# Kernel tuning notes

Measured on AMD Instinct MI355X. Metric: run time of the kernel, lower is better.

## Reference

```python
import jax, jax.numpy as jnp
from jax import lax
import numpy as np

V, D_EMB, H, P, B, T = 32000, 512, 1024, 512, 32, 512
NUM_LAYERS = 2


def setup_inputs() -> dict:
    key = jax.random.key(0)
    ks = jax.random.split(key, 2 + NUM_LAYERS * 5)
    tokens = jax.random.randint(ks[0], (B, T), 0, V, dtype=jnp.int32)
    embed = jax.random.normal(ks[1], (V, D_EMB), dtype=jnp.float32) * 0.02
    inp = {"tokens": tokens, "embed": embed}
    in_dims = [D_EMB] + [P] * (NUM_LAYERS - 1)
    for l in range(NUM_LAYERS):
        kk = ks[2 + 5 * l: 7 + 5 * l]
        inp[f"Wx{l}"] = jax.random.normal(kk[0], (in_dims[l], 4 * H), dtype=jnp.float32) * 0.02
        inp[f"Wh{l}"] = jax.random.normal(kk[1], (H, 4 * H), dtype=jnp.float32) * 0.02
        inp[f"b{l}"] = jnp.zeros((4 * H,), dtype=jnp.float32)
        inp[f"Wfc{l}"] = jax.random.normal(kk[3], (H, P), dtype=jnp.float32) * 0.02
        inp[f"bfc{l}"] = jnp.zeros((P,), dtype=jnp.float32)
    return inp


def _lstm(x, Wx, Wh, b):
    # x: [B, T, D] -> [B, T, H]. Keras gate order: i, f, g(cell), o.
    Bsz = x.shape[0]
    h0 = jnp.zeros((Bsz, H), dtype=x.dtype)
    c0 = jnp.zeros((Bsz, H), dtype=x.dtype)

    # Precompute input projection for all timesteps (one big GEMM).
    xz = jnp.einsum('btd,dg->btg', x, Wx) + b  # [B, T, 4H]

    def step(carry, zt):
        h, c = carry
        z = zt + h @ Wh
        i, f, g, o = jnp.split(z, 4, axis=-1)
        c = jax.nn.sigmoid(f) * c + jax.nn.sigmoid(i) * jnp.tanh(g)
        h = jax.nn.sigmoid(o) * jnp.tanh(c)
        return (h, c), h

    _, ys = lax.scan(step, (h0, c0), jnp.swapaxes(xz, 0, 1))  # ys: [T, B, H]
    return jnp.swapaxes(ys, 0, 1)


def reference(tokens, embed, Wx0, Wh0, b0, Wfc0, bfc0, Wx1, Wh1, b1, Wfc1, bfc1):
    # inference path: dropout is identity (training=False), use_softmax=False
    x = embed[tokens]  # [B, T, D_EMB]
    layers = [(Wx0, Wh0, b0, Wfc0, bfc0), (Wx1, Wh1, b1, Wfc1, bfc1)]
    for Wx, Wh, b, Wfc, bfc in layers:
        x = _lstm(x, Wx, Wh, b)
        x = x @ Wfc + bfc  # per-layer dense projection [B, T, P]
    return x
```

## Files before the change

kernel.cpp:

```cpp
#include <hip/hip_runtime.h>
#include <cstdio>
#include <cstdint>

typedef unsigned short u16;
typedef unsigned int u32;
typedef float f32x4 __attribute__((ext_vector_type(4)));
typedef short s16x8 __attribute__((ext_vector_type(8)));

#define DI __device__ __forceinline__

#define BATCH 32
#define SEQT 512
#define HDIM 1024
#define PDIM 512
#define DEMB 512
#define G4H 4096

DI u16 f2bf(float f) {
  u32 u = __float_as_uint(f);
  return (u16)((u + 0x7fffu + ((u >> 16) & 1u)) >> 16);
}
DI float bf2f(u16 h) { return __uint_as_float(((u32)h) << 16); }
DI void split2(float f, u16 &hi, u16 &lo) {
  hi = f2bf(f);
  lo = f2bf(f - bf2f(hi));
}
DI f32x4 mfma16(s16x8 a, s16x8 b, f32x4 c) {
  return __builtin_amdgcn_mfma_f32_16x16x32_bf16(a, b, c, 0, 0, 0);
}
DI void dma16(const void *g, void *l) {
  __builtin_amdgcn_global_load_lds((const __attribute__((address_space(1))) void *)g,
                                   (__attribute__((address_space(3))) void *)l, 16, 0, 0);
}
DI s16x8 ld128_dev(const u16 *p) {
  s16x8 r;
  asm volatile("global_load_dwordx4 %0, %1, off sc1" : "=v"(r) : "v"(p));
  return r;
}
DI f32x4 ldf4_dev(const float *p) {
  f32x4 r;
  asm volatile("global_load_dwordx4 %0, %1, off sc1" : "=v"(r) : "v"(p));
  return r;
}
DI void st16_dev(u16 *p, u16 v) {
  asm volatile("global_store_short %0, %1, off sc1" ::"v"(p), "v"((u32)v) : "memory");
}
DI void st32_dev(int *p, int v) {
  asm volatile("global_store_dword %0, %1, off sc1" ::"v"(p), "v"(v) : "memory");
}
DI void st128f_dev(float *p, f32x4 v) {
  asm volatile("global_store_dwordx4 %0, %1, off sc1" ::"v"(p), "v"(v) : "memory");
}

#if __has_builtin(__builtin_amdgcn_exp2f) && __has_builtin(__builtin_amdgcn_rcpf)
DI float fsig(float x) {
  return __builtin_amdgcn_rcpf(1.f + __builtin_amdgcn_exp2f(-1.4426950408889634f * x));
}
DI float ftanh(float x) {
  return 2.f * __builtin_amdgcn_rcpf(1.f + __builtin_amdgcn_exp2f(-2.8853900817779268f * x)) - 1.f;
}
#else
DI float fsig(float x) { return 1.f / (1.f + expf(-x)); }
DI float ftanh(float x) { return tanhf(x); }
#endif

__global__ void k_gather_pack(const int *__restrict__ tokens, const float *__restrict__ embed,
                              u16 *__restrict__ xhi, u16 *__restrict__ xlo) {
  int idx = blockIdx.x * 256 + threadIdx.x;
  int m = idx >> 6;
  int k8 = (idx & 63) << 3;
  int tok = tokens[m];
  const float *src = embed + (size_t)tok * DEMB + k8;
  float4 a = *(const float4 *)src;
  float4 b = *(const float4 *)(src + 4);
  float v[8] = {a.x, a.y, a.z, a.w, b.x, b.y, b.z, b.w};
  union UV { u16 h[8]; int4 v; };
  UV uh, ul;
#pragma unroll
  for (int j = 0; j < 8; ++j) split2(v[j], uh.h[j], ul.h[j]);
  size_t o = (size_t)m * DEMB + k8;
  *(int4 *)(xhi + o) = uh.v;
  *(int4 *)(xlo + o) = ul.v;
}

__global__ void k_packT(const float *__restrict__ W, u16 *__restrict__ Thi, u16 *__restrict__ Tlo,
                        int K, int N) {
  __shared__ float tile[32][33];
  int n0 = blockIdx.x * 32, k0 = blockIdx.y * 32;
  int tx = threadIdx.x, ty = threadIdx.y;
#pragma unroll
  for (int i = 0; i < 4; ++i) tile[ty + 8 * i][tx] = W[(size_t)(k0 + ty + 8 * i) * N + n0 + tx];
  __syncthreads();
#pragma unroll
  for (int i = 0; i < 4; ++i) {
    int n = ty + 8 * i;
    u16 hi, lo;
    split2(tile[tx][n], hi, lo);
    size_t o = (size_t)(n0 + n) * K + k0 + tx;
    Thi[o] = hi;
    Tlo[o] = lo;
  }
}

__global__ void k_split(const float *__restrict__ W, u16 *__restrict__ hi, u16 *__restrict__ lo,
                        int n) {
  int i = blockIdx.x * 256 + threadIdx.x;
  if (i < n) split2(W[i], hi[i], lo[i]);
}

__global__ void k_beff(const float *__restrict__ bfc0, const float *__restrict__ Wx1,
                       const float *__restrict__ b1, float *__restrict__ beff) {
  int n = blockIdx.x * 256 + threadIdx.x;
  float acc = b1[n];
  for (int j = 0; j < PDIM; ++j) acc += bfc0[j] * Wx1[(size_t)j * G4H + n];
  beff[n] = acc;
}

template <int OM, int SA>
__global__ __launch_bounds__(256, 2) void k_gemm(const u16 *__restrict__ Ahi, const u16 *__restrict__ Alo,
                                                 const u16 *__restrict__ Bhi, const u16 *__restrict__ Blo,
                                                 const float *__restrict__ bias, void *__restrict__ out0,
                                                 int M, int N, int K) {
  __shared__ u16 sP[4][128 * 64];
  const int tid = threadIdx.x;
  const int w = tid >> 6, lane = tid & 63;
  const int la15 = lane & 15, la4 = lane >> 4;
  const int nbn = N >> 7;
  const int bm = blockIdx.x / nbn, bn = blockIdx.x % nbn;
  const u16 *src = (w == 0) ? Ahi : (w == 1) ? Alo : (w == 2) ? Bhi : Blo;
  const int rowbase = (w < 2) ? bm * 128 : bn * 128;
  char *lds = (char *)&sP[w][0];

  if (SA) {
    for (int i = tid; i < 2048; i += 256) ((unsigned long long *)&sP[1][0])[i] = 0ULL;
  }

  f32x4 acc[2][8] = {};
  for (int kb = 0; kb < K; kb += 64) {
    if (!(SA && w == 1)) {
#pragma unroll
      for (int i = 0; i < 16; ++i) {
        int s = i * 64 + lane;
        int row = s >> 3;
        int k16 = (s & 7) ^ (row & 7);
        dma16(src + (size_t)(rowbase + row) * K + kb + k16 * 8, lds + i * 1024);
      }
    }
    asm volatile("s_waitcnt vmcnt(0)" ::: "memory");
    __syncthreads();
#pragma unroll
    for (int ksl = 0; ksl < 2; ++ksl) {
      s16x8 ah[2], al[2];
#pragma unroll
      for (int rf = 0; rf < 2; ++rf) {
        int row = 32 * w + 16 * rf + la15;
        int slot = row * 8 + ((4 * ksl + la4) ^ (row & 7));
        ah[rf] = *(const s16x8 *)((const char *)&sP[0][0] + slot * 16);
        al[rf] = *(const s16x8 *)((const char *)&sP[1][0] + slot * 16);
      }
#pragma unroll
      for (int cf = 0; cf < 8; ++cf) {
        int col = 16 * cf + la15;
        int slot = col * 8 + ((4 * ksl + la4) ^ (col & 7));
        s16x8 bh = *(const s16x8 *)((const char *)&sP[2][0] + slot * 16);
        s16x8 bl = *(const s16x8 *)((const char *)&sP[3][0] + slot * 16);
#pragma unroll
        for (int rf = 0; rf < 2; ++rf) {
          acc[rf][cf] = mfma16(ah[rf], bh, acc[rf][cf]);
          acc[rf][cf] = mfma16(ah[rf], bl, acc[rf][cf]);
          acc[rf][cf] = mfma16(al[rf], bh, acc[rf][cf]);
        }
      }
    }
    __syncthreads();
  }
#pragma unroll
  for (int rf = 0; rf < 2; ++rf) {
#pragma unroll
    for (int cf = 0; cf < 8; ++cf) {
      int c = bn * 128 + 16 * cf + la15;
      float bv = bias ? bias[c] : 0.f;
#pragma unroll
      for (int q = 0; q < 4; ++q) {
        int r = bm * 128 + 32 * w + 16 * rf + 4 * la4 + q;
        float v = acc[rf][cf][q] + bv;
        if (OM == 0) {
          ((u16 *)out0)[(size_t)r * N + c] = f2bf(v);
        } else {
          int b2 = r & 31, tt = r >> 5;
          ((float *)out0)[((size_t)b2 * SEQT + tt) * PDIM + c] = v;
        }
      }
    }
  }
}

__global__ __launch_bounds__(256, 1) void k_recur_pipe(
    const u16 *__restrict__ xz0, const float *__restrict__ Wh0, const float *__restrict__ Wh1,
    const u16 *__restrict__ Weff, const float *__restrict__ beff,
    u16 *h0h, u16 *h1h, float *zeffP, int *flags) {
  __shared__ u16 sW[32 * 1024];
  __shared__ u16 sE[32 * 1024];
  __shared__ float zacc[4][32][33];
  __shared__ float sC[256];
  __shared__ float zE[32][33];
  const int tid = threadIdx.x;
  const int w = tid >> 6, lane = tid & 63;
  const int la15 = lane & 15, la4 = lane >> 4;
  const int wg = blockIdx.x;
  const int layer = wg >> 7;
  const int g = wg & 127;

  const float *Wh = layer ? Wh1 : Wh0;
  for (int i2 = tid; i2 < 32 * 1024; i2 += 256) {
    int zc = i2 & 31;
    int k = i2 >> 5;
    int gcol = (zc >> 3) * HDIM + 8 * g + (zc & 7);
    int boff = zc * 2048 + ((((k >> 3) ^ (zc & 7))) << 4) + (k & 7) * 2;
    *(u16 *)((char *)sW + boff) = f2bf(Wh[(size_t)k * G4H + gcol]);
    if (!layer) *(u16 *)((char *)sE + boff) = Weff[(size_t)k * G4H + gcol];
  }
  sC[tid] = 0.f;
  __syncthreads();

  const int r_g = tid >> 3, hc = tid & 7;
  const int ks0 = 8 * w;

  if (!layer) {
    for (int t = 0; t <= SEQT; ++t) {
      const bool last = (t == SEQT);
      float xzv[4] = {0.f, 0.f, 0.f, 0.f};
      if (!last) {
        const u16 *px = xz0 + ((size_t)r_g * SEQT + t) * G4H + 8 * g + hc;
#pragma unroll
        for (int gi = 0; gi < 4; ++gi) xzv[gi] = bf2f(px[(size_t)gi * HDIM]);
      }
      if (w == 0 && t > 0) {
        const int *f0 = flags + lane;
        const int *f1 = flags + 128 + lane;
        const int bp = t - 16;
        for (long tries = 0;; ++tries) {
          int a = __hip_atomic_load(f0, __ATOMIC_RELAXED, __HIP_MEMORY_SCOPE_AGENT);
          int b = __hip_atomic_load(f0 + 64, __ATOMIC_RELAXED, __HIP_MEMORY_SCOPE_AGENT);
          bool ok = (a >= t && b >= t);
          if (t > 16) {
            int c = __hip_atomic_load(f1, __ATOMIC_RELAXED, __HIP_MEMORY_SCOPE_AGENT);
            int d = __hip_atomic_load(f1 + 64, __ATOMIC_RELAXED, __HIP_MEMORY_SCOPE_AGENT);
            ok = ok && (c >= bp && d >= bp);
          }
          if (__all(ok)) break;
          if (tries > (1L << 22)) break;
          __builtin_amdgcn_s_sleep(1);
        }
      }
      __syncthreads();
      if (t > 0) {
        const u16 *pA = h0h + (size_t)(t - 1) * 32 * HDIM;
        float *zb = zeffP + ((((size_t)((t - 1) & 15) * 128 + g) * 4 + w) << 10);
        s16x8 aw0[8], aw1[8];
#pragma unroll
        for (int j8 = 0; j8 < 8; ++j8)
          aw0[j8] = ld128_dev(pA + (size_t)la15 * HDIM + 32 * (ks0 + j8) + 8 * la4);
#pragma unroll
        for (int j8 = 0; j8 < 8; ++j8)
          aw1[j8] = ld128_dev(pA + (size_t)(16 + la15) * HDIM + 32 * (ks0 + j8) + 8 * la4);
        asm volatile("s_waitcnt vmcnt(0)" ::: "memory");
        __builtin_amdgcn_sched_barrier(0);
        {
          f32x4 acc0[2] = {}, accE[2] = {};
#pragma unroll
          for (int j8 = 0; j8 < 8; ++j8) {
#pragma unroll
            for (int cf = 0; cf < 2; ++cf) {
              int zc = 16 * cf + la15;
              int sl = (4 * (ks0 + j8) + la4) ^ (zc & 7);
              int boff = zc * 2048 + (sl << 4);
              if (!last) acc0[cf] = mfma16(aw0[j8], *(const s16x8 *)((const char *)sW + boff), acc0[cf]);
              accE[cf] = mfma16(aw0[j8], *(const s16x8 *)((const char *)sE + boff), accE[cf]);
            }
          }
#pragma unroll
          for (int cf = 0; cf < 2; ++cf) {
            if (!last) {
#pragma unroll
              for (int q = 0; q < 4; ++q) zacc[w][4 * la4 + q][16 * cf + la15] = acc0[cf][q];
            }
            st128f_dev(zb + (16 * cf + la15) * 32 + 4 * la4, accE[cf]);
          }
        }
        {
          f32x4 acc0[2] = {}, accE[2] = {};
#pragma unroll
          for (int j8 = 0; j8 < 8; ++j8) {
#pragma unroll
            for (int cf = 0; cf < 2; ++cf) {
              int zc = 16 * cf + la15;
              int sl = (4 * (ks0 + j8) + la4) ^ (zc & 7);
              int boff = zc * 2048 + (sl << 4);
              if (!last) acc0[cf] = mfma16(aw1[j8], *(const s16x8 *)((const char *)sW + boff), acc0[cf]);
              accE[cf] = mfma16(aw1[j8], *(const s16x8 *)((const char *)sE + boff), accE[cf]);
            }
          }
#pragma unroll
          for (int cf = 0; cf < 2; ++cf) {
            if (!last) {
#pragma unroll
              for (int q = 0; q < 4; ++q) zacc[w][16 + 4 * la4 + q][16 * cf + la15] = acc0[cf][q];
            }
            st128f_dev(zb + (16 * cf + la15) * 32 + 16 + 4 * la4, accE[cf]);
          }
        }
      }
      __syncthreads();
      if (!last) {
        float z4[4];
#pragma unroll
        for (int gi = 0; gi < 4; ++gi) {
          float s = xzv[gi];
          if (t > 0) {
            int zc = gi * 8 + hc;
            s += zacc[0][r_g][zc] + zacc[1][r_g][zc] + zacc[2][r_g][zc] + zacc[3][r_g][zc];
          }
          z4[gi] = s;
        }
        float ig = fsig(z4[0]);
        float fg = fsig(z4[1]);
        float gg = ftanh(z4[2]);
        float og = fsig(z4[3]);
        float c = fg * sC[tid] + ig * gg;
        sC[tid] = c;
        float h = og * ftanh(c);
        st16_dev(h0h + ((size_t)t * 32 + r_g) * HDIM + 8 * g + hc, f2bf(h));
      }
      asm volatile("s_waitcnt vmcnt(0)" ::: "memory");
      __syncthreads();
      if (tid == 0) st32_dev(flags + g, t + 1);
    }
  } else {
    float bef[4];
#pragma unroll
    for (int gi = 0; gi < 4; ++gi) bef[gi] = beff[gi * HDIM + 8 * g + hc];
    const int zc2 = tid >> 3, rowq = (tid & 7) << 2;
    for (int t = 0; t < SEQT; ++t) {
      if (w == 0) {
        const int *f0 = flags + lane;
        const int *f1 = flags + 128 + lane;
        const int need0 = t + 2;
        for (long tries = 0;; ++tries) {
          int a = __hip_atomic_load(f0, __ATOMIC_RELAXED, __HIP_MEMORY_SCOPE_AGENT);
          int b = __hip_atomic_load(f0 + 64, __ATOMIC_RELAXED, __HIP_MEMORY_SCOPE_AGENT);
          bool ok = (a >= need0 && b >= need0);
          if (t > 0) {
            int c = __hip_atomic_load(f1, __ATOMIC_RELAXED, __HIP_MEMORY_SCOPE_AGENT);
            int d = __hip_atomic_load(f1 + 64, __ATOMIC_RELAXED, __HIP_MEMORY_SCOPE_AGENT);
            ok = ok && (c >= t && d >= t);
          }
          if (__all(ok)) break;
          if (tries > (1L << 22)) break;
          __builtin_amdgcn_s_sleep(1);
        }
      }
      __syncthreads();
      s16x8 aw0[8], aw1[8];
      const u16 *pA = h1h + (size_t)(t - 1) * 32 * HDIM;
      if (t > 0) {
#pragma unroll
        for (int j8 = 0; j8 < 8; ++j8)
          aw0[j8] = ld128_dev(pA + (size_t)la15 * HDIM + 32 * (ks0 + j8) + 8 * la4);
#pragma unroll
        for (int j8 = 0; j8 < 8; ++j8)
          aw1[j8] = ld128_dev(pA + (size_t)(16 + la15) * HDIM + 32 * (ks0 + j8) + 8 * la4);
      }
      const float *rb0 = zeffP + (((size_t)(t & 15) * 128 + g) << 12);
      f32x4 zp0 = ldf4_dev(rb0 + zc2 * 32 + rowq);
      f32x4 zp1 = ldf4_dev(rb0 + 1024 + zc2 * 32 + rowq);
      f32x4 zp2 = ldf4_dev(rb0 + 2048 + zc2 * 32 + rowq);
      f32x4 zp3 = ldf4_dev(rb0 + 3072 + zc2 * 32 + rowq);
      asm volatile("s_waitcnt vmcnt(0)" ::: "memory");
      __builtin_amdgcn_sched_barrier(0);
      {
        f32x4 s4 = zp0 + zp1 + zp2 + zp3;
        zE[zc2][rowq + 0] = s4[0];
        zE[zc2][rowq + 1] = s4[1];
        zE[zc2][rowq + 2] = s4[2];
        zE[zc2][rowq + 3] = s4[3];
      }
      if (t > 0) {
        {
          f32x4 acc0[2] = {};
#pragma unroll
          for (int j8 = 0; j8 < 8; ++j8) {
#pragma unroll
            for (int cf = 0; cf < 2; ++cf) {
              int zc = 16 * cf + la15;
              int sl = (4 * (ks0 + j8) + la4) ^ (zc & 7);
              int boff = zc * 2048 + (sl << 4);
              acc0[cf] = mfma16(aw0[j8], *(const s16x8 *)((const char *)sW + boff), acc0[cf]);
            }
          }
#pragma unroll
          for (int cf = 0; cf < 2; ++cf)
#pragma unroll
            for (int q = 0; q < 4; ++q) zacc[w][4 * la4 + q][16 * cf + la15] = acc0[cf][q];
        }
        {
          f32x4 acc0[2] = {};
#pragma unroll
          for (int j8 = 0; j8 < 8; ++j8) {
#pragma unroll
            for (int cf = 0; cf < 2; ++cf) {
              int zc = 16 * cf + la15;
              int sl = (4 * (ks0 + j8) + la4) ^ (zc & 7);
              int boff = zc * 2048 + (sl << 4);
              acc0[cf] = mfma16(aw1[j8], *(const s16x8 *)((const char *)sW + boff), acc0[cf]);
            }
          }
#pragma unroll
          for (int cf = 0; cf < 2; ++cf)
#pragma unroll
            for (int q = 0; q < 4; ++q) zacc[w][16 + 4 * la4 + q][16 * cf + la15] = acc0[cf][q];
        }
      }
      __syncthreads();
      {
        float z4[4];
#pragma unroll
        for (int gi = 0; gi < 4; ++gi) {
          int zc = gi * 8 + hc;
          float s = bef[gi] + zE[zc][r_g];
          if (t > 0)
            s += zacc[0][r_g][zc] + zacc[1][r_g][zc] + zacc[2][r_g][zc] + zacc[3][r_g][zc];
          z4[gi] = s;
        }
        float ig = fsig(z4[0]);
        float fg = fsig(z4[1]);
        float gg = ftanh(z4[2]);
        float og = fsig(z4[3]);
        float c = fg * sC[tid] + ig * gg;
        sC[tid] = c;
        float h = og * ftanh(c);
        st16_dev(h1h + ((size_t)t * 32 + r_g) * HDIM + 8 * g + hc, f2bf(h));
      }
      asm volatile("s_waitcnt vmcnt(0)" ::: "memory");
      __syncthreads();
      if (tid == 0) st32_dev(flags + 128 + g, t + 1);
    }
  }
}

extern "C" void kernel_launch(void *const *d_in, const int *in_sizes, int n_in,
                              void *d_out, int out_size, void *d_ws, size_t ws_size,
                              hipStream_t stream) {
  const int *tokens = (const int *)d_in[0];
  const float *embed = (const float *)d_in[1];
  const float *Wx0 = (const float *)d_in[2];
  const float *Wh0 = (const float *)d_in[3];
  const float *b0 = (const float *)d_in[4];
  const float *Wfc0 = (const float *)d_in[5];
  const float *bfc0 = (const float *)d_in[6];
  const float *Wx1 = (const float *)d_in[7];
  const float *Wh1 = (const float *)d_in[8];
  const float *b1 = (const float *)d_in[9];
  const float *Wfc1 = (const float *)d_in[10];
  const float *bfc1 = (const float *)d_in[11];

  constexpr size_t NEED = 255856640;
  if (ws_size < NEED) {
    fprintf(stderr, "RNNLM kernel: ws too small (%zu < %zu)\n", ws_size, NEED);
    return;
  }
  char *ws = (char *)d_ws;
  u16 *xz0 = (u16 *)(ws + 0);
  u16 *h0h = (u16 *)(ws + 134217728);
  u16 *h1h = (u16 *)(ws + 167772160);
  u16 *x0hi = (u16 *)(ws + 201326592);
  u16 *x0lo = (u16 *)(ws + 218103808);
  u16 *Weff = (u16 *)(ws + 201326592);
  u16 *Wfc0hi = (u16 *)(ws + 209715200);
  u16 *Wfc0lo = (u16 *)(ws + 210763776);
  u16 *WfcT1hi = (u16 *)(ws + 211812352);
  u16 *WfcT1lo = (u16 *)(ws + 212860928);
  float *beff = (float *)(ws + 213909504);
  int *flags = (int *)(ws + 213925888);
  float *zeffP = (float *)(ws + 218103808);
  u16 *WxT0hi = (u16 *)(ws + 234881024);
  u16 *WxT0lo = (u16 *)(ws + 239075328);
  u16 *WxT1hi = (u16 *)(ws + 243269632);
  u16 *WxT1lo = (u16 *)(ws + 247463936);

  k_packT<<<dim3(G4H / 32, DEMB / 32), dim3(32, 8), 0, stream>>>(Wx0, WxT0hi, WxT0lo, DEMB, G4H);
  k_packT<<<dim3(G4H / 32, DEMB / 32), dim3(32, 8), 0, stream>>>(Wx1, WxT1hi, WxT1lo, DEMB, G4H);
  k_gather_pack<<<4096, 256, 0, stream>>>(tokens, embed, x0hi, x0lo);
  k_gemm<0, 0><<<dim3(128 * 32), 256, 0, stream>>>(x0hi, x0lo, WxT0hi, WxT0lo, b0, xz0,
                                                   16384, G4H, DEMB);
  k_split<<<2048, 256, 0, stream>>>(Wfc0, Wfc0hi, Wfc0lo, HDIM * PDIM);
  k_packT<<<dim3(PDIM / 32, HDIM / 32), dim3(32, 8), 0, stream>>>(Wfc1, WfcT1hi, WfcT1lo, HDIM, PDIM);
  k_beff<<<16, 256, 0, stream>>>(bfc0, Wx1, b1, beff);
  (void)hipMemsetAsync(flags, 0, 256 * sizeof(int), stream);
  k_gemm<0, 0><<<dim3(8 * 32), 256, 0, stream>>>(Wfc0hi, Wfc0lo, WxT1hi, WxT1lo, nullptr, Weff,
                                                 1024, G4H, PDIM);
  {
    const u16 *a0 = xz0; const float *a1 = Wh0; const float *a2 = Wh1;
    const u16 *a3 = Weff; const float *a4 = beff;
    u16 *a5 = h0h; u16 *a6 = h1h; float *a7 = zeffP; int *a8 = flags;
    void *args[] = {&a0, &a1, &a2, &a3, &a4, &a5, &a6, &a7, &a8};
    hipError_t e = hipLaunchCooperativeKernel((void *)k_recur_pipe, dim3(256), dim3(256), args, 0, stream);
    if (e != hipSuccess) fprintf(stderr, "coop launch failed: %d\n", (int)e);
  }
  k_gemm<2, 1><<<dim3(128 * 4), 256, 0, stream>>>(h1h, h1h, WfcT1hi, WfcT1lo, bfc1, d_out,
                                                  16384, PDIM, HDIM);
}
```

Before: 5.199 ms.

## Reduce layer-1 input projection in producer and pass it as packed bf16

```diff
diff --git a/kernel.cpp b/kernel.cpp
--- a/kernel.cpp
+++ b/kernel.cpp
@@ -6,6 +6,7 @@
 typedef unsigned int u32;
 typedef float f32x4 __attribute__((ext_vector_type(4)));
 typedef short s16x8 __attribute__((ext_vector_type(8)));
+typedef int i32x2 __attribute__((ext_vector_type(2)));
 
 #define DI __device__ __forceinline__
 
@@ -37,9 +38,9 @@
   asm volatile("global_load_dwordx4 %0, %1, off sc1" : "=v"(r) : "v"(p));
   return r;
 }
-DI f32x4 ldf4_dev(const float *p) {
-  f32x4 r;
-  asm volatile("global_load_dwordx4 %0, %1, off sc1" : "=v"(r) : "v"(p));
+DI i32x2 ld64_dev(const u16 *p) {
+  i32x2 r;
+  asm volatile("global_load_dwordx2 %0, %1, off sc1" : "=v"(r) : "v"(p));
   return r;
 }
 DI void st16_dev(u16 *p, u16 v) {
@@ -48,8 +49,8 @@
 DI void st32_dev(int *p, int v) {
   asm volatile("global_store_dword %0, %1, off sc1" ::"v"(p), "v"(v) : "memory");
 }
-DI void st128f_dev(float *p, f32x4 v) {
-  asm volatile("global_store_dwordx4 %0, %1, off sc1" ::"v"(p), "v"(v) : "memory");
+DI void st64_dev(u16 *p, i32x2 v) {
+  asm volatile("global_store_dwordx2 %0, %1, off sc1" ::"v"(p), "v"(v) : "memory");
 }
 
 #if __has_builtin(__builtin_amdgcn_exp2f) && __has_builtin(__builtin_amdgcn_rcpf)
@@ -198,12 +199,11 @@
 __global__ __launch_bounds__(256, 1) void k_recur_pipe(
     const u16 *__restrict__ xz0, const float *__restrict__ Wh0, const float *__restrict__ Wh1,
     const u16 *__restrict__ Weff, const float *__restrict__ beff,
-    u16 *h0h, u16 *h1h, float *zeffP, int *flags) {
+    u16 *h0h, u16 *h1h, u16 *zeffR, int *flags) {
   __shared__ u16 sW[32 * 1024];
   __shared__ u16 sE[32 * 1024];
   __shared__ float zacc[4][32][33];
   __shared__ float sC[256];
-  __shared__ float zE[32][33];
   const int tid = threadIdx.x;
   const int w = tid >> 6, lane = tid & 63;
   const int la15 = lane & 15, la4 = lane >> 4;
@@ -254,9 +254,9 @@
         }
       }
       __syncthreads();
+      f32x4 accE[2][2] = {};
       if (t > 0) {
         const u16 *pA = h0h + (size_t)(t - 1) * 32 * HDIM;
-        float *zb = zeffP + ((((size_t)((t - 1) & 15) * 128 + g) * 4 + w) << 10);
         s16x8 aw0[8], aw1[8];
 #pragma unroll
         for (int j8 = 0; j8 < 8; ++j8)
@@ -267,7 +267,7 @@
         asm volatile("s_waitcnt vmcnt(0)" ::: "memory");
         __builtin_amdgcn_sched_barrier(0);
         {
-          f32x4 acc0[2] = {}, accE[2] = {};
+          f32x4 acc0[2] = {};
 #pragma unroll
           for (int j8 = 0; j8 < 8; ++j8) {
 #pragma unroll
@@ -276,20 +276,18 @@
               int sl = (4 * (ks0 + j8) + la4) ^ (zc & 7);
               int boff = zc * 2048 + (sl << 4);
               if (!last) acc0[cf] = mfma16(aw0[j8], *(const s16x8 *)((const char *)sW + boff), acc0[cf]);
-              accE[cf] = mfma16(aw0[j8], *(const s16x8 *)((const char *)sE + boff), accE[cf]);
+              accE[0][cf] = mfma16(aw0[j8], *(const s16x8 *)((const char *)sE + boff), accE[0][cf]);
             }
           }
-#pragma unroll
-          for (int cf = 0; cf < 2; ++cf) {
-            if (!last) {
+          if (!last) {
+#pragma unroll
+            for (int cf = 0; cf < 2; ++cf)
 #pragma unroll
               for (int q = 0; q < 4; ++q) zacc[w][4 * la4 + q][16 * cf + la15] = acc0[cf][q];
-            }
-            st128f_dev(zb + (16 * cf + la15) * 32 + 4 * la4, accE[cf]);
           }
         }
         {
-          f32x4 acc0[2] = {}, accE[2] = {};
+          f32x4 acc0[2] = {};
 #pragma unroll
           for (int j8 = 0; j8 < 8; ++j8) {
 #pragma unroll
@@ -298,16 +296,14 @@
               int sl = (4 * (ks0 + j8) + la4) ^ (zc & 7);
               int boff = zc * 2048 + (sl << 4);
               if (!last) acc0[cf] = mfma16(aw1[j8], *(const s16x8 *)((const char *)sW + boff), acc0[cf]);
-              accE[cf] = mfma16(aw1[j8], *(const s16x8 *)((const char *)sE + boff), accE[cf]);
+              accE[1][cf] = mfma16(aw1[j8], *(const s16x8 *)((const char *)sE + boff), accE[1][cf]);
             }
           }
-#pragma unroll
-          for (int cf = 0; cf < 2; ++cf) {
-            if (!last) {
+          if (!last) {
+#pragma unroll
+            for (int cf = 0; cf < 2; ++cf)
 #pragma unroll
               for (int q = 0; q < 4; ++q) zacc[w][16 + 4 * la4 + q][16 * cf + la15] = acc0[cf][q];
-            }
-            st128f_dev(zb + (16 * cf + la15) * 32 + 16 + 4 * la4, accE[cf]);
           }
         }
       }
@@ -332,6 +328,29 @@
         float h = og * ftanh(c);
         st16_dev(h0h + ((size_t)t * 32 + r_g) * HDIM + 8 * g + hc, f2bf(h));
       }
+      __syncthreads();
+      if (t > 0) {
+#pragma unroll
+        for (int rt = 0; rt < 2; ++rt)
+#pragma unroll
+          for (int cf = 0; cf < 2; ++cf)
+#pragma unroll
+            for (int q = 0; q < 4; ++q)
+              zacc[w][16 * rt + 4 * la4 + q][16 * cf + la15] = accE[rt][cf][q];
+      }
+      __syncthreads();
+      if (t > 0) {
+        float ze[4];
+#pragma unroll
+        for (int gi = 0; gi < 4; ++gi) {
+          int zc = gi * 8 + hc;
+          ze[gi] = zacc[0][r_g][zc] + zacc[1][r_g][zc] + zacc[2][r_g][zc] + zacc[3][r_g][zc];
+        }
+        i32x2 pk;
+        pk[0] = (int)(((u32)f2bf(ze[1]) << 16) | (u32)f2bf(ze[0]));
+        pk[1] = (int)(((u32)f2bf(ze[3]) << 16) | (u32)f2bf(ze[2]));
+        st64_dev(zeffR + (((size_t)((t - 1) & 15) * 128 + g) << 10) + tid * 4, pk);
+      }
       asm volatile("s_waitcnt vmcnt(0)" ::: "memory");
       __syncthreads();
       if (tid == 0) st32_dev(flags + g, t + 1);
@@ -340,7 +359,6 @@
     float bef[4];
 #pragma unroll
     for (int gi = 0; gi < 4; ++gi) bef[gi] = beff[gi * HDIM + 8 * g + hc];
-    const int zc2 = tid >> 3, rowq = (tid & 7) << 2;
     for (int t = 0; t < SEQT; ++t) {
       if (w == 0) {
         const int *f0 = flags + lane;
@@ -371,20 +389,14 @@
         for (int j8 = 0; j8 < 8; ++j8)
           aw1[j8] = ld128_dev(pA + (size_t)(16 + la15) * HDIM + 32 * (ks0 + j8) + 8 * la4);
       }
-      const float *rb0 = zeffP + (((size_t)(t & 15) * 128 + g) << 12);
-      f32x4 zp0 = ldf4_dev(rb0 + zc2 * 32 + rowq);
-      f32x4 zp1 = ldf4_dev(rb0 + 1024 + zc2 * 32 + rowq);
-      f32x4 zp2 = ldf4_dev(rb0 + 2048 + zc2 * 32 + rowq);
-      f32x4 zp3 = ldf4_dev(rb0 + 3072 + zc2 * 32 + rowq);
+      i32x2 zpk = ld64_dev(zeffR + (((size_t)(t & 15) * 128 + g) << 10) + tid * 4);
       asm volatile("s_waitcnt vmcnt(0)" ::: "memory");
       __builtin_amdgcn_sched_barrier(0);
-      {
-        f32x4 s4 = zp0 + zp1 + zp2 + zp3;
-        zE[zc2][rowq + 0] = s4[0];
-        zE[zc2][rowq + 1] = s4[1];
-        zE[zc2][rowq + 2] = s4[2];
-        zE[zc2][rowq + 3] = s4[3];
-      }
+      float zv[4];
+      zv[0] = bf2f((u16)((u32)zpk[0] & 0xffffu));
+      zv[1] = bf2f((u16)((u32)zpk[0] >> 16));
+      zv[2] = bf2f((u16)((u32)zpk[1] & 0xffffu));
+      zv[3] = bf2f((u16)((u32)zpk[1] >> 16));
       if (t > 0) {
         {
           f32x4 acc0[2] = {};
@@ -426,10 +438,11 @@
         float z4[4];
 #pragma unroll
         for (int gi = 0; gi < 4; ++gi) {
-          int zc = gi * 8 + hc;
-          float s = bef[gi] + zE[zc][r_g];
-          if (t > 0)
+          float s = bef[gi] + zv[gi];
+          if (t > 0) {
+            int zc = gi * 8 + hc;
             s += zacc[0][r_g][zc] + zacc[1][r_g][zc] + zacc[2][r_g][zc] + zacc[3][r_g][zc];
+          }
           z4[gi] = s;
         }
         float ig = fsig(z4[0]);
@@ -482,7 +495,7 @@
   u16 *WfcT1lo = (u16 *)(ws + 212860928);
   float *beff = (float *)(ws + 213909504);
   int *flags = (int *)(ws + 213925888);
-  float *zeffP = (float *)(ws + 218103808);
+  u16 *zeffR = (u16 *)(ws + 218103808);
   u16 *WxT0hi = (u16 *)(ws + 234881024);
   u16 *WxT0lo = (u16 *)(ws + 239075328);
   u16 *WxT1hi = (u16 *)(ws + 243269632);
@@ -502,7 +515,7 @@
   {
     const u16 *a0 = xz0; const float *a1 = Wh0; const float *a2 = Wh1;
     const u16 *a3 = Weff; const float *a4 = beff;
-    u16 *a5 = h0h; u16 *a6 = h1h; float *a7 = zeffP; int *a8 = flags;
+    u16 *a5 = h0h; u16 *a6 = h1h; u16 *a7 = zeffR; int *a8 = flags;
     void *args[] = {&a0, &a1, &a2, &a3, &a4, &a5, &a6, &a7, &a8};
     hipError_t e = hipLaunchCooperativeKernel((void *)k_recur_pipe, dim3(256), dim3(256), args, 0, stream);
     if (e != hipSuccess) fprintf(stderr, "coop launch failed: %d\n", (int)e);
```

Result: no change. 5.151 ms (-0.9%).
